# Optimization experiments

Hardware: AMD Instinct MI355X
Metric: run time of the kernel (lower is better)

## Reference

```python
import jax, jax.numpy as jnp
import numpy as np

EMB = 768
HEADS = 12
HEAD_DIM = EMB // HEADS
SEQ = 4096
BATCH = 1


def setup_inputs() -> dict:
    key = jax.random.key(0)
    ks = jax.random.split(key, 9)
    s = 1.0 / np.sqrt(EMB)
    return {
        "x": jax.random.normal(ks[0], (BATCH, SEQ, EMB), dtype=jnp.float32),
        "wq": jax.random.normal(ks[1], (EMB, EMB), dtype=jnp.float32) * s,
        "bq": jax.random.normal(ks[2], (EMB,), dtype=jnp.float32) * s,
        "wk": jax.random.normal(ks[3], (EMB, EMB), dtype=jnp.float32) * s,
        "bk": jax.random.normal(ks[4], (EMB,), dtype=jnp.float32) * s,
        "wv": jax.random.normal(ks[5], (EMB, EMB), dtype=jnp.float32) * s,
        "bv": jax.random.normal(ks[6], (EMB,), dtype=jnp.float32) * s,
        "wo": jax.random.normal(ks[7], (EMB, EMB), dtype=jnp.float32) * s,
        "bo": jax.random.normal(ks[8], (EMB,), dtype=jnp.float32) * s,
    }


def reference(x, wq, bq, wk, bk, wv, bv, wo, bo):
    b, n, _ = x.shape
    # projections: [b, n, emb] -> [b, heads, n, head_dim]
    def split_heads(t):
        return t.reshape(b, n, HEADS, HEAD_DIM).transpose(0, 2, 1, 3)
    q = split_heads(x @ wq + bq)
    k = split_heads(x @ wk + bk)
    v = split_heads(x @ wv + bv)
    # full N x N scores (naive attention, as in the original)
    scores = jnp.einsum("bhqd,bhkd->bhqk", q, k)
    causal = jnp.triu(jnp.ones((n, n), dtype=bool), k=1)
    scores = jnp.where(causal, -jnp.inf, scores)
    weights = jax.nn.softmax(scores / np.sqrt(HEAD_DIM), axis=-1)
    # dropout with rate 0.0 is identity (eval mode)
    ctx = jnp.einsum("bhqk,bhkd->bhqd", weights, v)
    ctx = ctx.transpose(0, 2, 1, 3).reshape(b, n, EMB)
    return ctx @ wo + bo
```

## Files before the change

kernel.cpp:

```cpp
#include <hip/hip_runtime.h>
#include <stdint.h>

#define SEQ 4096
#define EMB 768
#define HEADS 12
#define HD 64

typedef __attribute__((ext_vector_type(8))) short short8;
typedef __attribute__((ext_vector_type(4))) short short4v;
typedef __attribute__((ext_vector_type(8))) __bf16 bf16x8;
typedef __attribute__((ext_vector_type(4))) __bf16 bf16x4;
typedef __attribute__((ext_vector_type(4))) float f32x4;

#define QSCALE 0.18033688011112043f

static __device__ __forceinline__ unsigned short f2bf(float f) {
    unsigned int u = __builtin_bit_cast(unsigned int, f);
    unsigned int r = 0x7fffu + ((u >> 16) & 1u);
    u += r;
    return (unsigned short)(u >> 16);
}

static __device__ __forceinline__ f32x4 mfma32(short8 a, short8 b, f32x4 c) {
    return __builtin_amdgcn_mfma_f32_16x16x32_bf16(
        __builtin_bit_cast(bf16x8, a), __builtin_bit_cast(bf16x8, b), c, 0, 0, 0);
}

static __device__ __forceinline__ f32x4 mfma16(short4v a, short4v b, f32x4 c) {
#if __has_builtin(__builtin_amdgcn_mfma_f32_16x16x16_bf16)
    return __builtin_amdgcn_mfma_f32_16x16x16_bf16(
        __builtin_bit_cast(bf16x4, a), __builtin_bit_cast(bf16x4, b), c, 0, 0, 0);
#else
    return __builtin_amdgcn_mfma_f32_16x16x16bf16_1k(a, b, c, 0, 0, 0);
#endif
}

static __device__ __forceinline__ short4v pack4bf(float a, float b, float c, float d) {
#if __has_builtin(__builtin_amdgcn_cvt_pk_bf16_f32)
    typedef __attribute__((ext_vector_type(2))) __bf16 bf16x2;
    bf16x2 lo = __builtin_amdgcn_cvt_pk_bf16_f32(a, b);
    bf16x2 hi = __builtin_amdgcn_cvt_pk_bf16_f32(c, d);
    uint2 u = {__builtin_bit_cast(unsigned int, lo), __builtin_bit_cast(unsigned int, hi)};
    return __builtin_bit_cast(short4v, u);
#else
    short4v p;
    p[0] = (short)f2bf(a); p[1] = (short)f2bf(b);
    p[2] = (short)f2bf(c); p[3] = (short)f2bf(d);
    return p;
#endif
}

static __device__ __forceinline__ void load_lds16(const void* g, void* l) {
    __builtin_amdgcn_global_load_lds(
        (const __attribute__((address_space(1))) unsigned int*)(uintptr_t)g,
        (__attribute__((address_space(3))) unsigned int*)(uintptr_t)l, 16, 0, 0);
}

static __device__ __forceinline__ int pid_of(int h, int i128, int ch) {
    int b = (i128 < 20) ? (i128 - 10)
                        : (i128 < 30 ? 10 + (i128 - 20) * 2 : 30 + (i128 - 30) * 3);
    return h * 36 + b + (ch - 1);
}

static __device__ __forceinline__ void softmax_step(f32x4* st, float& m_i, float& l_i,
                                                    f32x4* O, short4v* pk) {
    float t0 = fmaxf(fmaxf(st[0][0], st[0][1]), fmaxf(st[0][2], st[0][3]));
    float t1 = fmaxf(fmaxf(st[1][0], st[1][1]), fmaxf(st[1][2], st[1][3]));
    float t2 = fmaxf(fmaxf(st[2][0], st[2][1]), fmaxf(st[2][2], st[2][3]));
    float t3 = fmaxf(fmaxf(st[3][0], st[3][1]), fmaxf(st[3][2], st[3][3]));
    float mx = fmaxf(fmaxf(t0, t1), fmaxf(t2, t3));
    mx = fmaxf(mx, __shfl_xor(mx, 16));
    mx = fmaxf(mx, __shfl_xor(mx, 32));
    if (__ballot(mx > m_i + 5.0f)) {
        const bool inc = mx > m_i;
        const float mn = inc ? mx : m_i;
        const float alpha = __builtin_amdgcn_exp2f(m_i - mn);
        m_i = mn;
        l_i *= alpha;
        for (int dt = 0; dt < 4; dt++)
            for (int r = 0; r < 4; r++) O[dt][r] *= alpha;
    }
    float rs = 0.f;
    for (int nt = 0; nt < 4; nt++) {
        float p0 = __builtin_amdgcn_exp2f(st[nt][0] - m_i);
        float p1 = __builtin_amdgcn_exp2f(st[nt][1] - m_i);
        float p2 = __builtin_amdgcn_exp2f(st[nt][2] - m_i);
        float p3 = __builtin_amdgcn_exp2f(st[nt][3] - m_i);
        rs += p0 + p1 + p2 + p3;
        pk[nt] = pack4bf(p0, p1, p2, p3);
    }
    l_i += rs;
}

__global__ __launch_bounds__(256) void convert_all(const float* __restrict__ x,
                                                   const float* __restrict__ wq,
                                                   const float* __restrict__ wk,
                                                   const float* __restrict__ wv,
                                                   const float* __restrict__ wo,
                                                   unsigned short* __restrict__ xb,
                                                   unsigned short* __restrict__ wqkvT,
                                                   unsigned short* __restrict__ woT) {
    __shared__ float Ls[64][65];
    const int bid = blockIdx.x;
    if (bid < 3072) {
        int i = bid * 256 + threadIdx.x;
        float4 v = ((const float4*)x)[i];
        ushort4 o = {f2bf(v.x), f2bf(v.y), f2bf(v.z), f2bf(v.w)};
        ((ushort4*)xb)[i] = o;
        return;
    }
    const int idx = bid - 3072;
    const int z = idx / 144;
    const int bx = (idx % 144) / 12, by = idx % 12;
    const float* W = (z == 0) ? wq : (z == 1) ? wk : (z == 2) ? wv : wo;
    unsigned short* dst = (z < 3) ? (wqkvT + (size_t)z * EMB * EMB) : woT;
    const int k0 = bx * 64, n0 = by * 64;
    const int r = threadIdx.x >> 2, c0 = (threadIdx.x & 3) * 16;
    for (int j = 0; j < 16; j += 4) {
        float4 v = *(const float4*)&W[(size_t)(k0 + r) * EMB + n0 + c0 + j];
        Ls[r][c0 + j] = v.x;
        Ls[r][c0 + j + 1] = v.y;
        Ls[r][c0 + j + 2] = v.z;
        Ls[r][c0 + j + 3] = v.w;
    }
    __syncthreads();
    unsigned short tmp[16];
    for (int j = 0; j < 16; j++) tmp[j] = f2bf(Ls[c0 + j][r]);
    *(uint4*)&dst[(size_t)(n0 + r) * EMB + k0 + c0] = *(uint4*)tmp;
    *(uint4*)&dst[(size_t)(n0 + r) * EMB + k0 + c0 + 8] = *(uint4*)(tmp + 8);
}

__global__ __launch_bounds__(256) void gemm_qkv(const unsigned short* __restrict__ A,
                                                const unsigned short* __restrict__ Bt,
                                                const float* __restrict__ b0p,
                                                const float* __restrict__ b1p,
                                                const float* __restrict__ b2p,
                                                unsigned short* __restrict__ QKb,
                                                unsigned short* __restrict__ Vtb) {
    __shared__ __align__(16) unsigned short SMEM[16384];
    const int tid = threadIdx.x;
    const int wave = tid >> 6, lane = tid & 63, quad = lane >> 4, l16 = lane & 15;
    const int m0 = blockIdx.x * 128, n0 = blockIdx.y * 128;
    const int wm = (wave >> 1) * 64, wn = (wave & 1) * 64;
    const int lrow = lane >> 2, lcol = (lane & 3) * 8;

    f32x4 acc[4][4] = {};

    for (int t = 0; t < 2; t++) {
        int row = wave * 32 + t * 16 + lrow;
        load_lds16(&A[(size_t)(m0 + row) * EMB + lcol], &SMEM[(wave * 2 + t) * 512]);
        load_lds16(&Bt[(size_t)(n0 + row) * EMB + lcol], &SMEM[4096 + (wave * 2 + t) * 512]);
    }
    int buf = 0;
    for (int k0 = 0; k0 < EMB; k0 += 32) {
        __syncthreads();
        if (k0 + 32 < EMB) {
            unsigned short* A_ = &SMEM[(buf ^ 1) * 8192];
            unsigned short* B_ = A_ + 4096;
            for (int t = 0; t < 2; t++) {
                int row = wave * 32 + t * 16 + lrow;
                load_lds16(&A[(size_t)(m0 + row) * EMB + k0 + 32 + lcol], &A_[(wave * 2 + t) * 512]);
                load_lds16(&Bt[(size_t)(n0 + row) * EMB + k0 + 32 + lcol], &B_[(wave * 2 + t) * 512]);
            }
        }
        const unsigned short* A_ = &SMEM[buf * 8192];
        const unsigned short* B_ = A_ + 4096;
        short8 a[4], b[4];
        for (int i = 0; i < 4; i++) a[i] = *(const short8*)&A_[(wm + i * 16 + l16) * 32 + quad * 8];
        for (int i = 0; i < 4; i++) b[i] = *(const short8*)&B_[(wn + i * 16 + l16) * 32 + quad * 8];
        for (int i = 0; i < 4; i++)
            for (int j = 0; j < 4; j++) acc[i][j] = mfma32(a[i], b[j], acc[i][j]);
        buf ^= 1;
    }

    const int z = n0 / EMB;
    if (z < 2) {
        const float* bias = z ? b1p : b0p;
        const float sc = z ? 1.0f : QSCALE;
        for (int i = 0; i < 4; i++)
            for (int j = 0; j < 4; j++) {
                int mbase = m0 + wm + i * 16 + quad * 4;
                int n = n0 + wn + j * 16 + l16;
                float bv = bias[n - z * EMB];
                for (int r = 0; r < 4; r++)
                    QKb[(size_t)(mbase + r) * 1536 + n] = f2bf((acc[i][j][r] + bv) * sc);
            }
    } else {
        const int nn = n0 + wn + l16 - 2 * EMB;
        for (int j = 0; j < 4; j++) {
            __syncthreads();
            const float bv = b2p[nn + j * 16];
            const int nloc = (wave & 1) * 16 + l16;
            for (int i = 0; i < 4; i++) {
                ushort4 pk;
                pk.x = f2bf(acc[i][j][0] + bv);
                pk.y = f2bf(acc[i][j][1] + bv);
                pk.z = f2bf(acc[i][j][2] + bv);
                pk.w = f2bf(acc[i][j][3] + bv);
                *(ushort4*)&SMEM[nloc * 136 + wm + i * 16 + quad * 4] = pk;
            }
            __syncthreads();
            const int nl = tid >> 3, c = tid & 7;
            const int ng = (nl >> 4) * 64 + j * 16 + (nl & 15) + n0 - 2 * EMB;
            const int hh = ng >> 6, dd = ng & 63;
            unsigned short* dst = &Vtb[(size_t)(hh * HD + dd) * SEQ + m0];
            *(uint4*)&dst[c * 8] = *(uint4*)&SMEM[nl * 136 + c * 8];
            *(uint4*)&dst[64 + c * 8] = *(uint4*)&SMEM[nl * 136 + 64 + c * 8];
        }
    }
}

__global__ __launch_bounds__(256) void gemm_out(const unsigned short* __restrict__ A,
                                                const unsigned short* __restrict__ Bt,
                                                const float* __restrict__ bias,
                                                float* __restrict__ outp) {
    __shared__ __align__(16) unsigned short SMEM[12288];
    const int tid = threadIdx.x;
    const int wave = tid >> 6, lane = tid & 63, quad = lane >> 4, l16 = lane & 15;
    const int m0 = blockIdx.x * 64, n0 = blockIdx.y * 128;
    const int wm = (wave >> 1) * 32, wn = (wave & 1) * 64;
    const int lrow = lane >> 2, lcol = (lane & 3) * 8;

    f32x4 acc[2][4] = {};

    load_lds16(&A[(size_t)(m0 + wave * 16 + lrow) * EMB + lcol], &SMEM[wave * 512]);
    for (int t = 0; t < 2; t++) {
        int row = wave * 32 + t * 16 + lrow;
        load_lds16(&Bt[(size_t)(n0 + row) * EMB + lcol], &SMEM[4096 + (wave * 2 + t) * 512]);
    }
    int buf = 0;
    for (int k0 = 0; k0 < EMB; k0 += 32) {
        __syncthreads();
        if (k0 + 32 < EMB) {
            unsigned short* A_ = &SMEM[(buf ^ 1) * 2048];
            unsigned short* B_ = &SMEM[4096 + (buf ^ 1) * 4096];
            load_lds16(&A[(size_t)(m0 + wave * 16 + lrow) * EMB + k0 + 32 + lcol], &A_[wave * 512]);
            for (int t = 0; t < 2; t++) {
                int row = wave * 32 + t * 16 + lrow;
                load_lds16(&Bt[(size_t)(n0 + row) * EMB + k0 + 32 + lcol], &B_[(wave * 2 + t) * 512]);
            }
        }
        const unsigned short* A_ = &SMEM[buf * 2048];
        const unsigned short* B_ = &SMEM[4096 + buf * 4096];
        short8 a[2], b[4];
        for (int i = 0; i < 2; i++) a[i] = *(const short8*)&A_[(wm + i * 16 + l16) * 32 + quad * 8];
        for (int j = 0; j < 4; j++) b[j] = *(const short8*)&B_[(wn + j * 16 + l16) * 32 + quad * 8];
        for (int i = 0; i < 2; i++)
            for (int j = 0; j < 4; j++) acc[i][j] = mfma32(a[i], b[j], acc[i][j]);
        buf ^= 1;
    }

    for (int i = 0; i < 2; i++)
        for (int j = 0; j < 4; j++) {
            int mbase = m0 + wm + i * 16 + quad * 4;
            int n = n0 + wn + j * 16 + l16;
            float bv = bias[n];
            for (int r = 0; r < 4; r++) outp[(size_t)(mbase + r) * EMB + n] = acc[i][j][r] + bv;
        }
}

__global__ __launch_bounds__(256, 3) void attn_kernel(const unsigned short* __restrict__ QKb,
                                                      const unsigned short* __restrict__ Vtb,
                                                      unsigned short* __restrict__ ctxb,
                                                      unsigned short* __restrict__ Op,
                                                      float* __restrict__ mArr,
                                                      float* __restrict__ lArr) {
    __shared__ __align__(16) unsigned short Ks[2][64 * 64];
    __shared__ __align__(16) unsigned short Vs[2][64 * 64];

    const int bid = blockIdx.x;
    const int h = bid % HEADS;
    const int r2 = 67 - bid / HEADS;
    int i128, ch, nch;
    if (r2 < 10) {
        i128 = r2; ch = 0; nch = 1;
    } else if (r2 < 30) {
        int t = r2 - 10; i128 = 10 + (t >> 1); ch = t & 1; nch = 2;
    } else if (r2 < 60) {
        int t = r2 - 30; i128 = 20 + t / 3; ch = t % 3; nch = 3;
    } else {
        int t = r2 - 60; i128 = 30 + (t >> 2); ch = t & 3; nch = 4;
    }
    const int T = 2 * i128 + 2;
    const int kb = ch * T / nch;
    const int ke = (ch + 1) * T / nch - 1;
    const int qbase = i128 * 128;
    const int tid = threadIdx.x;
    const int wave = tid >> 6, lane = tid & 63, quad = lane >> 4, l16 = lane & 15;

    const unsigned short* Qg = QKb + (size_t)h * HD;
    const unsigned short* Kg = QKb + (size_t)(EMB + h * HD);
    const unsigned short* Vh = Vtb + (size_t)h * HD * SEQ;

    const int qa = qbase + wave * 32 + l16;
    const int qb = qa + 16;
    const short8 bQ0a = *(const short8*)&Qg[(size_t)qa * 1536 + quad * 8];
    const short8 bQ1a = *(const short8*)&Qg[(size_t)qa * 1536 + 32 + quad * 8];
    const short8 bQ0b = *(const short8*)&Qg[(size_t)qb * 1536 + quad * 8];
    const short8 bQ1b = *(const short8*)&Qg[(size_t)qb * 1536 + 32 + quad * 8];

    const int row = tid >> 2, t4 = tid & 3;
    const int swk = row & 7, swv = row & 15;

    f32x4 Oa[4] = {}, Ob[4] = {};
    float m_a = -3.0e38f, l_a = 0.f;
    float m_b = -3.0e38f, l_b = 0.f;

    uint4 kr0, kr1, vr0, vr1;
    {
        const int kb64 = kb * 64;
        const unsigned short* kp = &Kg[(size_t)(kb64 + row) * 1536];
        kr0 = *(const uint4*)&kp[(2 * t4) * 8];
        kr1 = *(const uint4*)&kp[(2 * t4 + 1) * 8];
        const unsigned short* vp = &Vh[(size_t)row * SEQ + kb64];
        vr0 = *(const uint4*)&vp[t4 * 16];
        vr1 = *(const uint4*)&vp[t4 * 16 + 8];
    }
    *(uint4*)&Ks[0][row * 64 + ((2 * t4) ^ swk) * 8] = kr0;
    *(uint4*)&Ks[0][row * 64 + ((2 * t4 + 1) ^ swk) * 8] = kr1;
    *(uint2*)&Vs[0][row * 64 + ((4 * t4) ^ swv) * 4] = ((const uint2*)&vr0)[0];
    *(uint2*)&Vs[0][row * 64 + ((4 * t4 + 1) ^ swv) * 4] = ((const uint2*)&vr0)[1];
    *(uint2*)&Vs[0][row * 64 + ((4 * t4 + 2) ^ swv) * 4] = ((const uint2*)&vr1)[0];
    *(uint2*)&Vs[0][row * 64 + ((4 * t4 + 3) ^ swv) * 4] = ((const uint2*)&vr1)[1];
    if (kb < ke) {
        const int nb = (kb + 1) * 64;
        const unsigned short* kp = &Kg[(size_t)(nb + row) * 1536];
        kr0 = *(const uint4*)&kp[(2 * t4) * 8];
        kr1 = *(const uint4*)&kp[(2 * t4 + 1) * 8];
        const unsigned short* vp = &Vh[(size_t)row * SEQ + nb];
        vr0 = *(const uint4*)&vp[t4 * 16];
        vr1 = *(const uint4*)&vp[t4 * 16 + 8];
    }
    __syncthreads();

    const int qw = qbase + wave * 32 + 31;
    int p = 0;
    for (int kt = kb; kt <= ke; kt++) {
        const int kbase = kt * 64;
        if (kt < ke) {
            const int pn = p ^ 1;
            *(uint4*)&Ks[pn][row * 64 + ((2 * t4) ^ swk) * 8] = kr0;
            *(uint4*)&Ks[pn][row * 64 + ((2 * t4 + 1) ^ swk) * 8] = kr1;
            *(uint2*)&Vs[pn][row * 64 + ((4 * t4) ^ swv) * 4] = ((const uint2*)&vr0)[0];
            *(uint2*)&Vs[pn][row * 64 + ((4 * t4 + 1) ^ swv) * 4] = ((const uint2*)&vr0)[1];
            *(uint2*)&Vs[pn][row * 64 + ((4 * t4 + 2) ^ swv) * 4] = ((const uint2*)&vr1)[0];
            *(uint2*)&Vs[pn][row * 64 + ((4 * t4 + 3) ^ swv) * 4] = ((const uint2*)&vr1)[1];
            if (kt + 1 < ke) {
                const int nb = (kt + 2) * 64;
                const unsigned short* kp = &Kg[(size_t)(nb + row) * 1536];
                kr0 = *(const uint4*)&kp[(2 * t4) * 8];
                kr1 = *(const uint4*)&kp[(2 * t4 + 1) * 8];
                const unsigned short* vp = &Vh[(size_t)row * SEQ + nb];
                vr0 = *(const uint4*)&vp[t4 * 16];
                vr1 = *(const uint4*)&vp[t4 * 16 + 8];
            }
        }

        if (kbase <= qw) {
            const int swr = l16 & 7;
            f32x4 sa[4], sb[4];
            for (int nt = 0; nt < 4; nt++) {
                short8 aK0 = *(const short8*)&Ks[p][(nt * 16 + l16) * 64 + (quad ^ swr) * 8];
                short8 aK1 = *(const short8*)&Ks[p][(nt * 16 + l16) * 64 + ((quad + 4) ^ swr) * 8];
                f32x4 za = {};
                za = mfma32(aK0, bQ0a, za);
                za = mfma32(aK1, bQ1a, za);
                sa[nt] = za;
                f32x4 zb = {};
                zb = mfma32(aK0, bQ0b, zb);
                zb = mfma32(aK1, bQ1b, zb);
                sb[nt] = zb;
            }
            if (kbase + 63 > qbase + wave * 32) {
                for (int nt = 0; nt < 4; nt++)
                    for (int r = 0; r < 4; r++) {
                        const int kk = kbase + nt * 16 + quad * 4 + r;
                        if (kk > qa) sa[nt][r] = -INFINITY;
                        if (kk > qb) sb[nt][r] = -INFINITY;
                    }
            }

            short4v pka[4], pkb[4];
            softmax_step(sa, m_a, l_a, Oa, pka);
            softmax_step(sb, m_b, l_b, Ob, pkb);

            for (int dt = 0; dt < 4; dt++)
                for (int nt = 0; nt < 4; nt++) {
                    short4v av =
                        *(const short4v*)&Vs[p][(dt * 16 + l16) * 64 + ((4 * nt + quad) ^ l16) * 4];
                    Oa[dt] = mfma16(av, pka[nt], Oa[dt]);
                    Ob[dt] = mfma16(av, pkb[nt], Ob[dt]);
                }
        }

        __syncthreads();
        p ^= 1;
    }

    l_a += __shfl_xor(l_a, 16);
    l_a += __shfl_xor(l_a, 32);
    l_b += __shfl_xor(l_b, 16);
    l_b += __shfl_xor(l_b, 32);

    const int qla = wave * 32 + l16;
    const int qlb = qla + 16;
    if (nch == 1) {
        const float ia = 1.f / l_a, ib = 1.f / l_b;
        for (int dt = 0; dt < 4; dt++) {
            ushort4 oa, ob;
            oa.x = f2bf(Oa[dt][0] * ia);
            oa.y = f2bf(Oa[dt][1] * ia);
            oa.z = f2bf(Oa[dt][2] * ia);
            oa.w = f2bf(Oa[dt][3] * ia);
            ob.x = f2bf(Ob[dt][0] * ib);
            ob.y = f2bf(Ob[dt][1] * ib);
            ob.z = f2bf(Ob[dt][2] * ib);
            ob.w = f2bf(Ob[dt][3] * ib);
            *(ushort4*)&ctxb[(size_t)qa * EMB + h * HD + dt * 16 + quad * 4] = oa;
            *(ushort4*)&ctxb[(size_t)qb * EMB + h * HD + dt * 16 + quad * 4] = ob;
        }
    } else {
        if (ch == 0) {
            for (int dt = 0; dt < 4; dt++) {
                ushort4 oa, ob;
                oa.x = f2bf(Oa[dt][0]);
                oa.y = f2bf(Oa[dt][1]);
                oa.z = f2bf(Oa[dt][2]);
                oa.w = f2bf(Oa[dt][3]);
                ob.x = f2bf(Ob[dt][0]);
                ob.y = f2bf(Ob[dt][1]);
                ob.z = f2bf(Ob[dt][2]);
                ob.w = f2bf(Ob[dt][3]);
                *(ushort4*)&ctxb[(size_t)qa * EMB + h * HD + dt * 16 + quad * 4] = oa;
                *(ushort4*)&ctxb[(size_t)qb * EMB + h * HD + dt * 16 + quad * 4] = ob;
            }
        } else {
            const int pid = pid_of(h, i128, ch);
            for (int dt = 0; dt < 4; dt++) {
                ushort4 oa, ob;
                oa.x = f2bf(Oa[dt][0]);
                oa.y = f2bf(Oa[dt][1]);
                oa.z = f2bf(Oa[dt][2]);
                oa.w = f2bf(Oa[dt][3]);
                ob.x = f2bf(Ob[dt][0]);
                ob.y = f2bf(Ob[dt][1]);
                ob.z = f2bf(Ob[dt][2]);
                ob.w = f2bf(Ob[dt][3]);
                *(ushort4*)&Op[(size_t)pid * 8192 + qla * 64 + dt * 16 + quad * 4] = oa;
                *(ushort4*)&Op[(size_t)pid * 8192 + qlb * 64 + dt * 16 + quad * 4] = ob;
            }
        }
        if (quad == 0) {
            const int mlb = ((h * 32 + i128) * 4 + ch) * 128;
            mArr[mlb + qla] = m_a;
            lArr[mlb + qla] = l_a;
            mArr[mlb + qlb] = m_b;
            lArr[mlb + qlb] = l_b;
        }
    }
}

__global__ __launch_bounds__(256) void merge_kernel(const unsigned short* __restrict__ Op,
                                                    const float* __restrict__ mArr,
                                                    const float* __restrict__ lArr,
                                                    unsigned short* __restrict__ ctxb) {
    const int gid = blockIdx.x;
    const int h = gid % HEADS;
    const int i128 = 10 + gid / HEADS;
    const int nch = (i128 < 20) ? 2 : (i128 < 30) ? 3 : 4;
    const int q = threadIdx.x >> 1, d0 = (threadIdx.x & 1) * 32;
    const int mlbase = (h * 32 + i128) * 4;

    float mc[4], lc[4];
    for (int c = 0; c < nch; c++) {
        mc[c] = mArr[(mlbase + c) * 128 + q];
        lc[c] = lArr[(mlbase + c) * 128 + q];
    }
    float M = mc[0];
    for (int c = 1; c < nch; c++) M = fmaxf(M, mc[c]);
    float w[4], L = 0.f;
    for (int c = 0; c < nch; c++) {
        w[c] = __builtin_amdgcn_exp2f(mc[c] - M);
        L += w[c] * lc[c];
    }
    const float inv = 1.f / L;
    for (int c = 0; c < nch; c++) w[c] *= inv;

    unsigned short* dst = &ctxb[(size_t)(i128 * 128 + q) * EMB + h * HD + d0];
    for (int jj = 0; jj < 32; jj += 8) {
        uint4 u0 = *(const uint4*)&dst[jj];
        float f[8];
        const unsigned short* p0 = (const unsigned short*)&u0;
        for (int t = 0; t < 8; t++)
            f[t] = w[0] * __builtin_bit_cast(float, (unsigned int)p0[t] << 16);
        for (int c = 1; c < nch; c++) {
            const int pid = pid_of(h, i128, c);
            uint4 u = *(const uint4*)&Op[(size_t)pid * 8192 + q * 64 + d0 + jj];
            const unsigned short* p = (const unsigned short*)&u;
            for (int t = 0; t < 8; t++)
                f[t] += w[c] * __builtin_bit_cast(float, (unsigned int)p[t] << 16);
        }
        unsigned short o[8];
        for (int t = 0; t < 8; t++) o[t] = f2bf(f[t]);
        *(uint4*)&dst[jj] = *(uint4*)o;
    }
}

extern "C" void kernel_launch(void* const* d_in, const int* in_sizes, int n_in,
                              void* d_out, int out_size, void* d_ws, size_t ws_size,
                              hipStream_t stream) {
    const float* x = (const float*)d_in[0];
    const float* wq = (const float*)d_in[1];
    const float* bq = (const float*)d_in[2];
    const float* wk = (const float*)d_in[3];
    const float* bk = (const float*)d_in[4];
    const float* wv = (const float*)d_in[5];
    const float* bv = (const float*)d_in[6];
    const float* wo = (const float*)d_in[7];
    const float* bo = (const float*)d_in[8];

    unsigned short* ws = (unsigned short*)d_ws;
    unsigned short* xb = ws;
    unsigned short* wqkvT = xb + SEQ * EMB;
    unsigned short* woT = wqkvT + 3 * EMB * EMB;
    unsigned short* QKb = woT + EMB * EMB;
    unsigned short* Vtb = QKb + (size_t)SEQ * 1536;
    unsigned short* ctxb = Vtb + HEADS * SEQ * HD;
    unsigned short* Op = xb;
    float* mArr = (float*)(ws + 3538944);
    float* lArr = mArr + 196608;

    convert_all<<<dim3(3072 + 576), 256, 0, stream>>>(x, wq, wk, wv, wo, xb, wqkvT, woT);
    gemm_qkv<<<dim3(SEQ / 128, 3 * EMB / 128), 256, 0, stream>>>(
        xb, wqkvT, bq, bk, bv, QKb, Vtb);
    attn_kernel<<<dim3(12 * 68), 256, 0, stream>>>(QKb, Vtb, ctxb, Op, mArr, lArr);
    merge_kernel<<<dim3(264), 256, 0, stream>>>(Op, mArr, lArr, ctxb);
    gemm_out<<<dim3(SEQ / 64, EMB / 128), 256, 0, stream>>>(ctxb, woT, bo, (float*)d_out);
}
```

Measured before the change: 186.3 us.

## Software-pipeline QK^T of next key tile with softmax and PV of current

```diff
diff --git a/kernel.cpp b/kernel.cpp
--- a/kernel.cpp
+++ b/kernel.cpp
@@ -62,16 +62,16 @@
     return h * 36 + b + (ch - 1);
 }
 
-static __device__ __forceinline__ void softmax_step(f32x4* st, float& m_i, float& l_i,
-                                                    f32x4* O, short4v* pk) {
+static __device__ __forceinline__ void softmax_q(f32x4* st, float& m_i, float& l_i,
+                                                 f32x4* O, short4v* pk) {
     float t0 = fmaxf(fmaxf(st[0][0], st[0][1]), fmaxf(st[0][2], st[0][3]));
     float t1 = fmaxf(fmaxf(st[1][0], st[1][1]), fmaxf(st[1][2], st[1][3]));
     float t2 = fmaxf(fmaxf(st[2][0], st[2][1]), fmaxf(st[2][2], st[2][3]));
     float t3 = fmaxf(fmaxf(st[3][0], st[3][1]), fmaxf(st[3][2], st[3][3]));
     float mx = fmaxf(fmaxf(t0, t1), fmaxf(t2, t3));
-    mx = fmaxf(mx, __shfl_xor(mx, 16));
-    mx = fmaxf(mx, __shfl_xor(mx, 32));
     if (__ballot(mx > m_i + 5.0f)) {
+        mx = fmaxf(mx, __shfl_xor(mx, 16));
+        mx = fmaxf(mx, __shfl_xor(mx, 32));
         const bool inc = mx > m_i;
         const float mn = inc ? mx : m_i;
         const float alpha = __builtin_amdgcn_exp2f(m_i - mn);
@@ -265,7 +265,7 @@
                                                       unsigned short* __restrict__ Op,
                                                       float* __restrict__ mArr,
                                                       float* __restrict__ lArr) {
-    __shared__ __align__(16) unsigned short Ks[2][64 * 64];
+    __shared__ __align__(16) unsigned short Ks[64 * 64];
     __shared__ __align__(16) unsigned short Vs[2][64 * 64];
 
     const int bid = blockIdx.x;
@@ -316,8 +316,8 @@
         vr0 = *(const uint4*)&vp[t4 * 16];
         vr1 = *(const uint4*)&vp[t4 * 16 + 8];
     }
-    *(uint4*)&Ks[0][row * 64 + ((2 * t4) ^ swk) * 8] = kr0;
-    *(uint4*)&Ks[0][row * 64 + ((2 * t4 + 1) ^ swk) * 8] = kr1;
+    *(uint4*)&Ks[row * 64 + ((2 * t4) ^ swk) * 8] = kr0;
+    *(uint4*)&Ks[row * 64 + ((2 * t4 + 1) ^ swk) * 8] = kr1;
     *(uint2*)&Vs[0][row * 64 + ((4 * t4) ^ swv) * 4] = ((const uint2*)&vr0)[0];
     *(uint2*)&Vs[0][row * 64 + ((4 * t4 + 1) ^ swv) * 4] = ((const uint2*)&vr0)[1];
     *(uint2*)&Vs[0][row * 64 + ((4 * t4 + 2) ^ swv) * 4] = ((const uint2*)&vr1)[0];
@@ -334,17 +334,42 @@
     __syncthreads();
 
     const int qw = qbase + wave * 32 + 31;
+    const int swr = l16 & 7;
+
+    f32x4 sa[4], sb[4];
+    if (kb * 64 <= qw) {
+        for (int nt = 0; nt < 4; nt++) {
+            short8 aK0 = *(const short8*)&Ks[(nt * 16 + l16) * 64 + (quad ^ swr) * 8];
+            short8 aK1 = *(const short8*)&Ks[(nt * 16 + l16) * 64 + ((quad + 4) ^ swr) * 8];
+            f32x4 za = {};
+            za = mfma32(aK0, bQ0a, za);
+            za = mfma32(aK1, bQ1a, za);
+            sa[nt] = za;
+            f32x4 zb = {};
+            zb = mfma32(aK0, bQ0b, zb);
+            zb = mfma32(aK1, bQ1b, zb);
+            sb[nt] = zb;
+        }
+        if (kb * 64 + 63 > qbase + wave * 32) {
+            for (int nt = 0; nt < 4; nt++)
+                for (int r = 0; r < 4; r++) {
+                    const int kk = kb * 64 + nt * 16 + quad * 4 + r;
+                    if (kk > qa) sa[nt][r] = -INFINITY;
+                    if (kk > qb) sb[nt][r] = -INFINITY;
+                }
+        }
+    }
+
     int p = 0;
     for (int kt = kb; kt <= ke; kt++) {
-        const int kbase = kt * 64;
+        __syncthreads();
         if (kt < ke) {
-            const int pn = p ^ 1;
-            *(uint4*)&Ks[pn][row * 64 + ((2 * t4) ^ swk) * 8] = kr0;
-            *(uint4*)&Ks[pn][row * 64 + ((2 * t4 + 1) ^ swk) * 8] = kr1;
-            *(uint2*)&Vs[pn][row * 64 + ((4 * t4) ^ swv) * 4] = ((const uint2*)&vr0)[0];
-            *(uint2*)&Vs[pn][row * 64 + ((4 * t4 + 1) ^ swv) * 4] = ((const uint2*)&vr0)[1];
-            *(uint2*)&Vs[pn][row * 64 + ((4 * t4 + 2) ^ swv) * 4] = ((const uint2*)&vr1)[0];
-            *(uint2*)&Vs[pn][row * 64 + ((4 * t4 + 3) ^ swv) * 4] = ((const uint2*)&vr1)[1];
+            *(uint4*)&Ks[row * 64 + ((2 * t4) ^ swk) * 8] = kr0;
+            *(uint4*)&Ks[row * 64 + ((2 * t4 + 1) ^ swk) * 8] = kr1;
+            *(uint2*)&Vs[p ^ 1][row * 64 + ((4 * t4) ^ swv) * 4] = ((const uint2*)&vr0)[0];
+            *(uint2*)&Vs[p ^ 1][row * 64 + ((4 * t4 + 1) ^ swv) * 4] = ((const uint2*)&vr0)[1];
+            *(uint2*)&Vs[p ^ 1][row * 64 + ((4 * t4 + 2) ^ swv) * 4] = ((const uint2*)&vr1)[0];
+            *(uint2*)&Vs[p ^ 1][row * 64 + ((4 * t4 + 3) ^ swv) * 4] = ((const uint2*)&vr1)[1];
             if (kt + 1 < ke) {
                 const int nb = (kt + 2) * 64;
                 const unsigned short* kp = &Kg[(size_t)(nb + row) * 1536];
@@ -355,13 +380,22 @@
                 vr1 = *(const uint4*)&vp[t4 * 16 + 8];
             }
         }
-
-        if (kbase <= qw) {
-            const int swr = l16 & 7;
-            f32x4 sa[4], sb[4];
+        __syncthreads();
+
+        const int kbase = kt * 64;
+        const bool cur = (kbase <= qw);
+
+        short4v pka[4], pkb[4];
+        if (cur) {
+            softmax_q(sa, m_a, l_a, Oa, pka);
+            softmax_q(sb, m_b, l_b, Ob, pkb);
+        }
+
+        const int kn = kbase + 64;
+        if (kt < ke && kn <= qw) {
             for (int nt = 0; nt < 4; nt++) {
-                short8 aK0 = *(const short8*)&Ks[p][(nt * 16 + l16) * 64 + (quad ^ swr) * 8];
-                short8 aK1 = *(const short8*)&Ks[p][(nt * 16 + l16) * 64 + ((quad + 4) ^ swr) * 8];
+                short8 aK0 = *(const short8*)&Ks[(nt * 16 + l16) * 64 + (quad ^ swr) * 8];
+                short8 aK1 = *(const short8*)&Ks[(nt * 16 + l16) * 64 + ((quad + 4) ^ swr) * 8];
                 f32x4 za = {};
                 za = mfma32(aK0, bQ0a, za);
                 za = mfma32(aK1, bQ1a, za);
@@ -371,19 +405,17 @@
                 zb = mfma32(aK1, bQ1b, zb);
                 sb[nt] = zb;
             }
-            if (kbase + 63 > qbase + wave * 32) {
+            if (kn + 63 > qbase + wave * 32) {
                 for (int nt = 0; nt < 4; nt++)
                     for (int r = 0; r < 4; r++) {
-                        const int kk = kbase + nt * 16 + quad * 4 + r;
+                        const int kk = kn + nt * 16 + quad * 4 + r;
                         if (kk > qa) sa[nt][r] = -INFINITY;
                         if (kk > qb) sb[nt][r] = -INFINITY;
                     }
             }
-
-            short4v pka[4], pkb[4];
-            softmax_step(sa, m_a, l_a, Oa, pka);
-            softmax_step(sb, m_b, l_b, Ob, pkb);
-
+        }
+
+        if (cur) {
             for (int dt = 0; dt < 4; dt++)
                 for (int nt = 0; nt < 4; nt++) {
                     short4v av =
@@ -393,7 +425,6 @@
                 }
         }
 
-        __syncthreads();
         p ^= 1;
     }
 
```

Measured after the change: 183.0 us. About the same (-1.7%).
